# Kernel optimization log

Measured on AMD Instinct MI355X. Metric: run time of the kernel, lower is better.

## Reference

```python
import jax, jax.numpy as jnp
import numpy as np

B, S, I, H, O, L = 64, 1024, 128, 512, 128, 2

def _gru_layer(x, h0, Wzx, Wzh, bz, Wrx, Wrh, br, Wgx, Wgh, bg):
    # Precompute input projections for all timesteps: (B,S,H)
    xz = jnp.einsum('bsi,ih->bsh', x, Wzx)
    xr = jnp.einsum('bsi,ih->bsh', x, Wrx)
    xg = jnp.einsum('bsi,ih->bsh', x, Wgx)
    def step(h, inp):
        xz_t, xr_t, xg_t = inp
        z = jax.nn.sigmoid(xz_t + h @ Wzh + bz)
        r = jax.nn.sigmoid(xr_t + h @ Wrh + br)
        g = jnp.tanh(xg_t + (r * h) @ Wgh + bg)
        h_new = z * h + (1.0 - z) * g
        return h_new, h_new
    # scan over time: move S to leading axis
    xs = (jnp.swapaxes(xz, 0, 1), jnp.swapaxes(xr, 0, 1), jnp.swapaxes(xg, 0, 1))
    hT, ys = jax.lax.scan(step, h0, xs)
    return jnp.swapaxes(ys, 0, 1), hT  # (B,S,H), (B,H)

def setup_inputs() -> dict:
    key = jax.random.key(0)
    ks = jax.random.split(key, 32)
    d = {}
    d['input'] = jax.random.normal(ks[0], (B, S, I), dtype=jnp.float32)
    d['hidden_state'] = jnp.zeros((B, L, H), dtype=jnp.float32)
    kidx = 1
    for layer in range(L):
        din = I if layer == 0 else H
        sx = 1.0 / np.sqrt(din)
        sh = 1.0 / np.sqrt(H)
        for gate in ('z', 'r', 'g'):
            d[f'W{gate}x{layer}'] = jax.random.uniform(ks[kidx], (din, H), jnp.float32, -sx, sx); kidx += 1
            d[f'W{gate}h{layer}'] = jax.random.uniform(ks[kidx], (H, H), jnp.float32, -sh, sh); kidx += 1
            d[f'b{gate}{layer}'] = jax.random.uniform(ks[kidx], (H,), jnp.float32, -sh, sh); kidx += 1
    so = 1.0 / np.sqrt(H)
    d['Wout'] = jax.random.uniform(ks[kidx], (H, O), jnp.float32, -so, so); kidx += 1
    d['bout'] = jax.random.uniform(ks[kidx], (O,), jnp.float32, -so, so)
    return d

def reference(input, hidden_state,
              Wzx0, Wzh0, bz0, Wrx0, Wrh0, br0, Wgx0, Wgh0, bg0,
              Wzx1, Wzh1, bz1, Wrx1, Wrh1, br1, Wgx1, Wgh1, bg1,
              Wout, bout):
    params = [
        (Wzx0, Wzh0, bz0, Wrx0, Wrh0, br0, Wgx0, Wgh0, bg0),
        (Wzx1, Wzh1, bz1, Wrx1, Wrh1, br1, Wgx1, Wgh1, bg1),
    ]
    x = input
    finals = []
    for layer in range(L):
        h0 = hidden_state[:, layer, :]
        x, hT = _gru_layer(x, h0, *params[layer])
        finals.append(hT)
    layer_output = jnp.einsum('bsh,ho->bso', x, Wout) + bout  # (B,S,O)
    hidden_out = jnp.stack(finals, axis=1)  # (B,L,H)
    return layer_output, hidden_out
```

## Files before the change

### kernel.cpp

```cpp
#include <hip/hip_runtime.h>
#include <cstdint>
#include <cstddef>

#define BDIM 256
#define NWG  256

constexpr int B_ = 64, S_ = 1024, I_ = 128, H_ = 512, O_ = 128;
constexpr size_t HB = (size_t)H_ * B_;

constexpr size_t Y1_OFF  = 0;
constexpr size_t Y2_OFF  = Y1_OFF + 2 * HB;
constexpr size_t RH0_OFF = Y2_OFF + 2 * HB;
constexpr size_t RH1_OFF = RH0_OFF + HB;
constexpr size_t Z0_OFF  = RH1_OFF + HB;
constexpr size_t Z1_OFF  = Z0_OFF + HB;
constexpr size_t BAR_OFF = Z1_OFF + HB;
constexpr size_t BAR_WORDS = 34 * 64;
constexpr size_t SLAB_TOT = BAR_OFF + BAR_WORDS;
constexpr size_t XT_OFF  = SLAB_TOT;
constexpr size_t XT_FLOATS = (size_t)S_ * I_ * B_;
constexpr size_t WS_NEED_XT_BYTES = (XT_OFF + XT_FLOATS) * 4;

__device__ __forceinline__ float4 llc_load4(const float* p) {
  const unsigned long long* q = (const unsigned long long*)p;
  unsigned long long lo = __hip_atomic_load(q,     __ATOMIC_RELAXED, __HIP_MEMORY_SCOPE_AGENT);
  unsigned long long hi = __hip_atomic_load(q + 1, __ATOMIC_RELAXED, __HIP_MEMORY_SCOPE_AGENT);
  union { unsigned long long u[2]; float4 v; } c;
  c.u[0] = lo; c.u[1] = hi;
  return c.v;
}
__device__ __forceinline__ float llc_loadf(const float* p) {
  unsigned int u = __hip_atomic_load((const unsigned int*)p, __ATOMIC_RELAXED,
                                     __HIP_MEMORY_SCOPE_AGENT);
  union { unsigned int u; float f; } c; c.u = u;
  return c.f;
}
__device__ __forceinline__ void llc_storef(float* p, float x) {
  union { float f; unsigned int u; } c; c.f = x;
  __hip_atomic_store((unsigned int*)p, c.u, __ATOMIC_RELAXED, __HIP_MEMORY_SCOPE_AGENT);
}

__global__ void k_init(const float* __restrict__ hidden, float* __restrict__ ws) {
  int idx = blockIdx.x * 256 + threadIdx.x;
  if (idx < (int)(2 * HB)) {
    int l = idx >> 15, r = idx & 32767;
    int k = r >> 6, b = r & 63;
    ws[(l ? Y2_OFF : Y1_OFF) + HB + r] = hidden[b * 1024 + l * 512 + k];
  } else if (idx < (int)(2 * HB + BAR_WORDS)) {
    ((unsigned int*)(ws + BAR_OFF))[idx - 2 * HB] = 0u;
  }
}

__global__ void k_transpose_x(const float* __restrict__ in, float* __restrict__ Xt) {
  const size_t NQ = (size_t)B_ * S_ * I_ / 4;
  for (size_t q = (size_t)blockIdx.x * blockDim.x + threadIdx.x; q < NQ;
       q += (size_t)gridDim.x * blockDim.x) {
    int i4 = (int)(q & 31);
    int t  = (int)((q >> 5) & 1023);
    int b  = (int)(q >> 15);
    float4 v = *(const float4*)(in + ((size_t)b * 1024 + t) * 128 + i4 * 4);
    float* dst = Xt + (size_t)t * 8192 + (size_t)(i4 * 4) * 64 + b;
    dst[0] = v.x; dst[64] = v.y; dst[128] = v.z; dst[192] = v.w;
  }
}

__device__ __forceinline__ void fmas(float4& a, float s, const float4 h) {
  a.x = fmaf(s, h.x, a.x); a.y = fmaf(s, h.y, a.y);
  a.z = fmaf(s, h.z, a.z); a.w = fmaf(s, h.w, a.w);
}

__device__ __forceinline__ void dotA8(const float* __restrict__ src, const float* __restrict__ wAp,
                                      int kt, int b4, float4* acc) {
  #pragma unroll 8
  for (int ch = 0; ch < 32; ++ch) {
    int kk = ch * 16 + kt;
    float4 h = llc_load4(src + (size_t)kk * 64 + b4);
    const float* wp = wAp + kk * 8;
    float4 w0 = *(const float4*)wp;
    float4 w1 = *(const float4*)(wp + 4);
    fmas(acc[0], w0.x, h); fmas(acc[1], w0.y, h); fmas(acc[2], w0.z, h); fmas(acc[3], w0.w, h);
    fmas(acc[4], w1.x, h); fmas(acc[5], w1.y, h); fmas(acc[6], w1.z, h); fmas(acc[7], w1.w, h);
  }
}

__device__ __forceinline__ void fusedL1r1(const float* __restrict__ src,
                                          const float* __restrict__ wAp,
                                          const float* __restrict__ wBp,
                                          int kt, int b4, float4* acc, float4* accB) {
  #pragma unroll 8
  for (int ch = 0; ch < 32; ++ch) {
    int kk = ch * 16 + kt;
    float4 h = llc_load4(src + (size_t)kk * 64 + b4);
    const float* wp = wAp + kk * 8;
    float4 w0 = *(const float4*)wp;
    float4 w1 = *(const float4*)(wp + 4);
    fmas(acc[0], w0.x, h); fmas(acc[1], w0.y, h); fmas(acc[2], w0.z, h); fmas(acc[3], w0.w, h);
    fmas(acc[4], w1.x, h); fmas(acc[5], w1.y, h); fmas(acc[6], w1.z, h); fmas(acc[7], w1.w, h);
    const float* gp = wBp + kk * 4;
    float4 g0 = *(const float4*)gp;
    fmas(accB[0], g0.x, h); fmas(accB[1], g0.y, h); fmas(accB[2], g0.z, h); fmas(accB[3], g0.w, h);
  }
}

__device__ __forceinline__ void fusedL1r2(const float* __restrict__ src,
                                          const float* __restrict__ wAp2,
                                          const float* __restrict__ wOp,
                                          int kt, int b4, float4* acc, float4& accO) {
  #pragma unroll 8
  for (int ch = 0; ch < 32; ++ch) {
    int kk = ch * 16 + kt;
    float4 h = llc_load4(src + (size_t)kk * 64 + b4);
    const float* wp = wAp2 + kk * 8;
    float4 w0 = *(const float4*)wp;
    float4 w1 = *(const float4*)(wp + 4);
    fmas(acc[0], w0.x, h); fmas(acc[1], w0.y, h); fmas(acc[2], w0.z, h); fmas(acc[3], w0.w, h);
    fmas(acc[4], w1.x, h); fmas(acc[5], w1.y, h); fmas(acc[6], w1.z, h); fmas(acc[7], w1.w, h);
    fmas(accO, wOp[kk], h);
  }
}

__device__ __forceinline__ void fusedL0x(const float* __restrict__ src,
                                         const float* __restrict__ wAp2,
                                         const float* __restrict__ wBp2,
                                         int kt, int b4, float4* acc, float4* accB) {
  #pragma unroll 8
  for (int ch = 0; ch < 8; ++ch) {
    int i = ch * 16 + kt;
    float4 h = *(const float4*)(src + (size_t)i * 64 + b4);
    const float* wp = wAp2 + i * 8;
    float4 w0 = *(const float4*)wp;
    float4 w1 = *(const float4*)(wp + 4);
    fmas(acc[0], w0.x, h); fmas(acc[1], w0.y, h); fmas(acc[2], w0.z, h); fmas(acc[3], w0.w, h);
    fmas(acc[4], w1.x, h); fmas(acc[5], w1.y, h); fmas(acc[6], w1.z, h); fmas(acc[7], w1.w, h);
    const float* gp = wBp2 + i * 4;
    float4 g0 = *(const float4*)gp;
    fmas(accB[0], g0.x, h); fmas(accB[1], g0.y, h); fmas(accB[2], g0.z, h); fmas(accB[3], g0.w, h);
  }
}

__device__ __forceinline__ void fusedL0xf(const float* __restrict__ xin, int tau,
                                          const float* __restrict__ wAp2,
                                          const float* __restrict__ wBp2,
                                          int kt, int b4, float4* acc, float4* accB) {
  #pragma unroll 2
  for (int ch = 0; ch < 8; ++ch) {
    int i = ch * 16 + kt;
    float4 h;
    h.x = xin[(size_t)(b4 + 0) * 131072 + tau * 128 + i];
    h.y = xin[(size_t)(b4 + 1) * 131072 + tau * 128 + i];
    h.z = xin[(size_t)(b4 + 2) * 131072 + tau * 128 + i];
    h.w = xin[(size_t)(b4 + 3) * 131072 + tau * 128 + i];
    const float* wp = wAp2 + i * 8;
    float4 w0 = *(const float4*)wp;
    float4 w1 = *(const float4*)(wp + 4);
    fmas(acc[0], w0.x, h); fmas(acc[1], w0.y, h); fmas(acc[2], w0.z, h); fmas(acc[3], w0.w, h);
    fmas(acc[4], w1.x, h); fmas(acc[5], w1.y, h); fmas(acc[6], w1.z, h); fmas(acc[7], w1.w, h);
    const float* gp = wBp2 + i * 4;
    float4 g0 = *(const float4*)gp;
    fmas(accB[0], g0.x, h); fmas(accB[1], g0.y, h); fmas(accB[2], g0.z, h); fmas(accB[3], g0.w, h);
  }
}

__device__ __forceinline__ void dotB4(const float* __restrict__ src, const float* __restrict__ wBp,
                                      int kt, int b4, float4* acc) {
  #pragma unroll 8
  for (int ch = 0; ch < 32; ++ch) {
    int kk = ch * 16 + kt;
    float4 h = llc_load4(src + (size_t)kk * 64 + b4);
    const float* wp = wBp + kk * 4;
    float4 w0 = *(const float4*)wp;
    fmas(acc[0], w0.x, h); fmas(acc[1], w0.y, h); fmas(acc[2], w0.z, h); fmas(acc[3], w0.w, h);
  }
}

__device__ __forceinline__ void grid_barrier(unsigned int* bar, unsigned int ph) {
  __syncthreads();
  asm volatile("" ::: "memory");
  if (threadIdx.x == 0) {
    const int g = (int)(blockIdx.x >> 4);
    unsigned int* grp_cnt  = bar + (size_t)g * 64;
    unsigned int* root_cnt = bar + 16 * 64;
    unsigned int* grp_gen  = bar + (size_t)(17 + g) * 64;
    unsigned int* root_gen = bar + 33 * 64;
    unsigned int r = __hip_atomic_fetch_add(grp_cnt, 1u, __ATOMIC_RELAXED, __HIP_MEMORY_SCOPE_AGENT);
    if (r == 16u * ph - 1u) {
      unsigned int rr = __hip_atomic_fetch_add(root_cnt, 1u, __ATOMIC_RELAXED, __HIP_MEMORY_SCOPE_AGENT);
      if (rr == 16u * ph - 1u) {
        __hip_atomic_store(root_gen, ph, __ATOMIC_RELAXED, __HIP_MEMORY_SCOPE_AGENT);
      } else {
        while (__hip_atomic_load(root_gen, __ATOMIC_RELAXED, __HIP_MEMORY_SCOPE_AGENT) < ph)
          __builtin_amdgcn_s_sleep(1);
      }
      __hip_atomic_store(grp_gen, ph, __ATOMIC_RELAXED, __HIP_MEMORY_SCOPE_AGENT);
    } else {
      while (__hip_atomic_load(grp_gen, __ATOMIC_RELAXED, __HIP_MEMORY_SCOPE_AGENT) < ph)
        __builtin_amdgcn_s_sleep(1);
    }
  }
  asm volatile("" ::: "memory");
  __syncthreads();
}

struct ScanArgs {
  float* ws;
  const float* xin;
  float* out;
  const float *Wzx0, *Wzh0, *bz0, *Wrx0, *Wrh0, *br0, *Wgx0, *Wgh0, *bg0;
  const float *Wzx1, *Wzh1, *bz1, *Wrx1, *Wrh1, *br1, *Wgx1, *Wgh1, *bg1;
  const float *Wout, *bout;
  int use_xt;
};

__launch_bounds__(BDIM, 1)
__global__ void k_scan(ScanArgs a) {
  float* ws = a.ws;
  unsigned int* bar = (unsigned int*)(ws + BAR_OFF);

  const int tid = threadIdx.x;
  const int wg  = blockIdx.x;
  const int kt  = tid >> 4;
  const int bq  = tid & 15;
  const int b4  = bq << 2;

  const int mA  = wg >> 6;
  const int lA  = mA >> 1;
  const int gA  = mA & 1;
  const int jA0 = (wg & 63) * 8;
  const int KA  = (mA < 2) ? 640 : 1024;
  const int mB  = wg >> 7;
  const int jB0 = (wg & 127) * 4;
  const int KB  = mB ? 1024 : 640;
  const int oc  = wg - 128;

  __shared__ float wA[8192];
  __shared__ float wB[4096];
  __shared__ float wO[512];
  __shared__ float pA[9 * 64 * 17];

  {
    const float* A0 = lA ? (gA ? a.Wrx1 : a.Wzx1) : (gA ? a.Wrh0 : a.Wzh0);
    const float* A1 = lA ? (gA ? a.Wrh1 : a.Wzh1) : (gA ? a.Wrx0 : a.Wzx0);
    for (int idx = tid; idx < KA * 8; idx += BDIM) {
      int k = idx >> 3, c = idx & 7;
      wA[idx] = (k < 512) ? A0[k * 512 + jA0 + c] : A1[(k - 512) * 512 + jA0 + c];
    }
    const float* B0 = mB ? a.Wgx1 : a.Wgh0;
    const float* B1 = mB ? a.Wgh1 : a.Wgx0;
    for (int idx = tid; idx < KB * 4; idx += BDIM) {
      int k = idx >> 2, c = idx & 3;
      wB[idx] = (k < 512) ? B0[k * 512 + jB0 + c] : B1[(k - 512) * 512 + jB0 + c];
    }
    if (wg >= 128)
      for (int idx = tid; idx < 512; idx += BDIM) wO[idx] = a.Wout[(size_t)idx * 128 + oc];
  }
  const float* bAv = lA ? (gA ? a.br1 : a.bz1) : (gA ? a.br0 : a.bz0);
  const float biasA_0 = bAv[jA0 + (tid >> 6)];
  const float biasA_1 = bAv[jA0 + 4 + (tid >> 6)];
  const float biasB_0 = (mB ? a.bg1 : a.bg0)[jB0 + (tid >> 6)];
  const float boutW = (wg >= 128) ? a.bout[oc] : 0.f;
  __syncthreads();

  const float* XT = ws + XT_OFF;
  unsigned int ph = 1;

  for (int tau = 0; tau <= S_ + 1; ++tau) {
    const bool doL0 = (tau < S_);
    const bool doL1 = (tau >= 1) && (tau <= S_);
    const int slotP = (tau + 1) & 1;
    const int slotQ = tau & 1;
    const float* y1p = ws + Y1_OFF + (size_t)slotP * HB;
    const float* y2p = ws + Y2_OFF + (size_t)slotQ * HB;
    float* y1w = ws + Y1_OFF + (size_t)slotQ * HB;
    float* y2w = ws + Y2_OFF + (size_t)slotP * HB;

    const bool actA = lA ? doL1 : doL0;
    const bool doOut = (tau >= 2) && (wg >= 128);
    float4 acc[8];
    float4 accB[4];
    float4 accO = make_float4(0.f, 0.f, 0.f, 0.f);
    #pragma unroll
    for (int c = 0; c < 8; ++c) acc[c] = make_float4(0.f, 0.f, 0.f, 0.f);
    #pragma unroll
    for (int c = 0; c < 4; ++c) accB[c] = make_float4(0.f, 0.f, 0.f, 0.f);

    if (actA) {
      if (mA < 2) {
        dotA8(y1p, wA, kt, b4, acc);
        if (a.use_xt) fusedL0x(XT + (size_t)tau * 8192, wA + 512 * 8, wB + 512 * 4, kt, b4, acc, accB);
        else          fusedL0xf(a.xin, tau, wA + 512 * 8, wB + 512 * 4, kt, b4, acc, accB);
      } else {
        fusedL1r1(y1p, wA, wB, kt, b4, acc, accB);
        fusedL1r2(y2p, wA + 512 * 8, wO, kt, b4, acc, accO);
      }
    } else if (tau == S_ + 1 && wg >= 128) {
      #pragma unroll 8
      for (int ch = 0; ch < 32; ++ch) {
        int kk = ch * 16 + kt;
        float4 h = llc_load4(y2p + (size_t)kk * 64 + b4);
        fmas(accO, wO[kk], h);
      }
    }

    if (actA) {
      #pragma unroll
      for (int c = 0; c < 8; ++c) {
        float pv[4] = {acc[c].x, acc[c].y, acc[c].z, acc[c].w};
        #pragma unroll
        for (int j = 0; j < 4; ++j) pA[(c * 64 + b4 + j) * 17 + kt] = pv[j];
      }
    }
    if (doOut) {
      float pv[4] = {accO.x, accO.y, accO.z, accO.w};
      #pragma unroll
      for (int j = 0; j < 4; ++j) pA[(512 + b4 + j) * 17 + kt] = pv[j];
    }
    __syncthreads();
    if (actA) {
      #pragma unroll
      for (int r = 0; r < 2; ++r) {
        int idx = tid + (r << 8);
        int c = idx >> 6, b = idx & 63;
        float s = r ? biasA_1 : biasA_0;
        #pragma unroll
        for (int q = 0; q < 16; ++q) s += pA[(c * 64 + b) * 17 + q];
        float v = 1.0f / (1.0f + __expf(-s));
        size_t jb = (size_t)(jA0 + c) * 64 + b;
        if (gA == 0) {
          llc_storef(ws + (lA ? Z1_OFF : Z0_OFF) + jb, v);
        } else {
          const float* hpsl = lA ? y2p : y1p;
          float hp = llc_loadf(hpsl + jb);
          llc_storef(ws + (lA ? RH1_OFF : RH0_OFF) + jb, v * hp);
        }
      }
    }
    if (doOut && tid < 64) {
      float s = boutW;
      #pragma unroll
      for (int q = 0; q < 16; ++q) s += pA[(512 + tid) * 17 + q];
      a.out[((size_t)tid * 1024 + (tau - 2)) * 128 + oc] = s;
    }

    grid_barrier(bar, ph++);

    const bool actB = mB ? doL1 : doL0;
    if (actB) {
      if (mB == 0) dotB4(ws + RH0_OFF, wB, kt, b4, accB);
      else         dotB4(ws + RH1_OFF, wB + 512 * 4, kt, b4, accB);
      #pragma unroll
      for (int c = 0; c < 4; ++c) {
        float pv[4] = {accB[c].x, accB[c].y, accB[c].z, accB[c].w};
        #pragma unroll
        for (int j = 0; j < 4; ++j) pA[(c * 64 + b4 + j) * 17 + kt] = pv[j];
      }
    }
    __syncthreads();
    if (actB) {
      int c = tid >> 6, b = tid & 63;
      float s = biasB_0;
      #pragma unroll
      for (int q = 0; q < 16; ++q) s += pA[(c * 64 + b) * 17 + q];
      float g = tanhf(s);
      size_t jb = (size_t)(jB0 + c) * 64 + b;
      float z  = llc_loadf(ws + (mB ? Z1_OFF : Z0_OFF) + jb);
      float hp = llc_loadf((mB ? y2p : y1p) + jb);
      float hn = fmaf(z, hp - g, g);
      llc_storef((mB ? y2w : y1w) + jb, hn);
    }

    grid_barrier(bar, ph++);
  }
}

__global__ void k_hidden(const float* __restrict__ ws, float* __restrict__ out) {
  int idx = blockIdx.x * 256 + threadIdx.x;
  int b = idx >> 10, rem = idx & 1023, l = rem >> 9, j = rem & 511;
  const float* src = ws + (l ? Y2_OFF : Y1_OFF) + HB + (size_t)j * 64 + b;
  out[(size_t)B_ * S_ * O_ + idx] = *src;
}

extern "C" void kernel_launch(void* const* d_in, const int* in_sizes, int n_in,
                              void* d_out, int out_size, void* d_ws, size_t ws_size,
                              hipStream_t stream) {
  const float* input  = (const float*)d_in[0];
  const float* hidden = (const float*)d_in[1];
  const float* Wzx0 = (const float*)d_in[2],  *Wzh0 = (const float*)d_in[3],  *bz0 = (const float*)d_in[4];
  const float* Wrx0 = (const float*)d_in[5],  *Wrh0 = (const float*)d_in[6],  *br0 = (const float*)d_in[7];
  const float* Wgx0 = (const float*)d_in[8],  *Wgh0 = (const float*)d_in[9],  *bg0 = (const float*)d_in[10];
  const float* Wzx1 = (const float*)d_in[11], *Wzh1 = (const float*)d_in[12], *bz1 = (const float*)d_in[13];
  const float* Wrx1 = (const float*)d_in[14], *Wrh1 = (const float*)d_in[15], *br1 = (const float*)d_in[16];
  const float* Wgx1 = (const float*)d_in[17], *Wgh1 = (const float*)d_in[18], *bg1 = (const float*)d_in[19];
  const float* Wout = (const float*)d_in[20], *bout = (const float*)d_in[21];
  float* ws = (float*)d_ws;
  float* out = (float*)d_out;

  const int use_xt = (ws_size >= WS_NEED_XT_BYTES) ? 1 : 0;

  k_init<<<265, BDIM, 0, stream>>>(hidden, ws);
  if (use_xt) k_transpose_x<<<2048, BDIM, 0, stream>>>(input, ws + XT_OFF);

  ScanArgs sa{ws, input, out,
              Wzx0, Wzh0, bz0, Wrx0, Wrh0, br0, Wgx0, Wgh0, bg0,
              Wzx1, Wzh1, bz1, Wrx1, Wrh1, br1, Wgx1, Wgh1, bg1,
              Wout, bout, use_xt};
  k_scan<<<dim3(NWG), dim3(BDIM), 0, stream>>>(sa);

  k_hidden<<<256, 256, 0, stream>>>(ws, out);
}
```

Measured before the change: 18.28 ms.

## Double scan workgroup threads and pre-reduce K-split partials with wave shuffles

```diff
diff --git a/kernel.cpp b/kernel.cpp
--- a/kernel.cpp
+++ b/kernel.cpp
@@ -2,7 +2,8 @@
 #include <cstdint>
 #include <cstddef>
 
-#define BDIM 256
+#define BDIM 512
+#define ABLK 256
 #define NWG  256
 
 constexpr int B_ = 64, S_ = 1024, I_ = 128, H_ = 512, O_ = 128;
@@ -41,7 +42,7 @@
 }
 
 __global__ void k_init(const float* __restrict__ hidden, float* __restrict__ ws) {
-  int idx = blockIdx.x * 256 + threadIdx.x;
+  int idx = blockIdx.x * ABLK + threadIdx.x;
   if (idx < (int)(2 * HB)) {
     int l = idx >> 15, r = idx & 32767;
     int k = r >> 6, b = r & 63;
@@ -72,8 +73,8 @@
 __device__ __forceinline__ void dotA8(const float* __restrict__ src, const float* __restrict__ wAp,
                                       int kt, int b4, float4* acc) {
   #pragma unroll 8
-  for (int ch = 0; ch < 32; ++ch) {
-    int kk = ch * 16 + kt;
+  for (int ch = 0; ch < 16; ++ch) {
+    int kk = ch * 32 + kt;
     float4 h = llc_load4(src + (size_t)kk * 64 + b4);
     const float* wp = wAp + kk * 8;
     float4 w0 = *(const float4*)wp;
@@ -88,8 +89,8 @@
                                           const float* __restrict__ wBp,
                                           int kt, int b4, float4* acc, float4* accB) {
   #pragma unroll 8
-  for (int ch = 0; ch < 32; ++ch) {
-    int kk = ch * 16 + kt;
+  for (int ch = 0; ch < 16; ++ch) {
+    int kk = ch * 32 + kt;
     float4 h = llc_load4(src + (size_t)kk * 64 + b4);
     const float* wp = wAp + kk * 8;
     float4 w0 = *(const float4*)wp;
@@ -107,8 +108,8 @@
                                           const float* __restrict__ wOp,
                                           int kt, int b4, float4* acc, float4& accO) {
   #pragma unroll 8
-  for (int ch = 0; ch < 32; ++ch) {
-    int kk = ch * 16 + kt;
+  for (int ch = 0; ch < 16; ++ch) {
+    int kk = ch * 32 + kt;
     float4 h = llc_load4(src + (size_t)kk * 64 + b4);
     const float* wp = wAp2 + kk * 8;
     float4 w0 = *(const float4*)wp;
@@ -123,9 +124,9 @@
                                          const float* __restrict__ wAp2,
                                          const float* __restrict__ wBp2,
                                          int kt, int b4, float4* acc, float4* accB) {
-  #pragma unroll 8
-  for (int ch = 0; ch < 8; ++ch) {
-    int i = ch * 16 + kt;
+  #pragma unroll 4
+  for (int ch = 0; ch < 4; ++ch) {
+    int i = ch * 32 + kt;
     float4 h = *(const float4*)(src + (size_t)i * 64 + b4);
     const float* wp = wAp2 + i * 8;
     float4 w0 = *(const float4*)wp;
@@ -143,8 +144,8 @@
                                           const float* __restrict__ wBp2,
                                           int kt, int b4, float4* acc, float4* accB) {
   #pragma unroll 2
-  for (int ch = 0; ch < 8; ++ch) {
-    int i = ch * 16 + kt;
+  for (int ch = 0; ch < 4; ++ch) {
+    int i = ch * 32 + kt;
     float4 h;
     h.x = xin[(size_t)(b4 + 0) * 131072 + tau * 128 + i];
     h.y = xin[(size_t)(b4 + 1) * 131072 + tau * 128 + i];
@@ -164,13 +165,21 @@
 __device__ __forceinline__ void dotB4(const float* __restrict__ src, const float* __restrict__ wBp,
                                       int kt, int b4, float4* acc) {
   #pragma unroll 8
-  for (int ch = 0; ch < 32; ++ch) {
-    int kk = ch * 16 + kt;
+  for (int ch = 0; ch < 16; ++ch) {
+    int kk = ch * 32 + kt;
     float4 h = llc_load4(src + (size_t)kk * 64 + b4);
     const float* wp = wBp + kk * 4;
     float4 w0 = *(const float4*)wp;
     fmas(acc[0], w0.x, h); fmas(acc[1], w0.y, h); fmas(acc[2], w0.z, h); fmas(acc[3], w0.w, h);
   }
+}
+
+__device__ __forceinline__ float4 wave_red4(float4 v) {
+  v.x += __shfl_down(v.x, 32); v.y += __shfl_down(v.y, 32);
+  v.z += __shfl_down(v.z, 32); v.w += __shfl_down(v.w, 32);
+  v.x += __shfl_down(v.x, 16); v.y += __shfl_down(v.y, 16);
+  v.z += __shfl_down(v.z, 16); v.w += __shfl_down(v.w, 16);
+  return v;
 }
 
 __device__ __forceinline__ void grid_barrier(unsigned int* bar, unsigned int ph) {
@@ -221,6 +230,8 @@
   const int kt  = tid >> 4;
   const int bq  = tid & 15;
   const int b4  = bq << 2;
+  const int ktg = kt >> 2;
+  const bool strl = ((kt & 3) == 0);
 
   const int mA  = wg >> 6;
   const int lA  = mA >> 1;
@@ -235,7 +246,7 @@
   __shared__ float wA[8192];
   __shared__ float wB[4096];
   __shared__ float wO[512];
-  __shared__ float pA[9 * 64 * 17];
+  __shared__ float pA[9 * 64 * 9];
 
   {
     const float* A0 = lA ? (gA ? a.Wrx1 : a.Wzx1) : (gA ? a.Wrh0 : a.Wzh0);
@@ -254,9 +265,8 @@
       for (int idx = tid; idx < 512; idx += BDIM) wO[idx] = a.Wout[(size_t)idx * 128 + oc];
   }
   const float* bAv = lA ? (gA ? a.br1 : a.bz1) : (gA ? a.br0 : a.bz0);
-  const float biasA_0 = bAv[jA0 + (tid >> 6)];
-  const float biasA_1 = bAv[jA0 + 4 + (tid >> 6)];
-  const float biasB_0 = (mB ? a.bg1 : a.bg0)[jB0 + (tid >> 6)];
+  const float biasA = bAv[jA0 + (tid >> 6)];
+  const float biasB = (tid < 256) ? (mB ? a.bg1 : a.bg0)[jB0 + (tid >> 6)] : 0.f;
   const float boutW = (wg >= 128) ? a.bout[oc] : 0.f;
   __syncthreads();
 
@@ -294,8 +304,8 @@
       }
     } else if (tau == S_ + 1 && wg >= 128) {
       #pragma unroll 8
-      for (int ch = 0; ch < 32; ++ch) {
-        int kk = ch * 16 + kt;
+      for (int ch = 0; ch < 16; ++ch) {
+        int kk = ch * 32 + kt;
         float4 h = llc_load4(y2p + (size_t)kk * 64 + b4);
         fmas(accO, wO[kk], h);
       }
@@ -304,40 +314,44 @@
     if (actA) {
       #pragma unroll
       for (int c = 0; c < 8; ++c) {
-        float pv[4] = {acc[c].x, acc[c].y, acc[c].z, acc[c].w};
-        #pragma unroll
-        for (int j = 0; j < 4; ++j) pA[(c * 64 + b4 + j) * 17 + kt] = pv[j];
+        float4 v = wave_red4(acc[c]);
+        if (strl) {
+          pA[(c * 64 + b4 + 0) * 9 + ktg] = v.x;
+          pA[(c * 64 + b4 + 1) * 9 + ktg] = v.y;
+          pA[(c * 64 + b4 + 2) * 9 + ktg] = v.z;
+          pA[(c * 64 + b4 + 3) * 9 + ktg] = v.w;
+        }
       }
     }
     if (doOut) {
-      float pv[4] = {accO.x, accO.y, accO.z, accO.w};
-      #pragma unroll
-      for (int j = 0; j < 4; ++j) pA[(512 + b4 + j) * 17 + kt] = pv[j];
+      float4 v = wave_red4(accO);
+      if (strl) {
+        pA[(512 + b4 + 0) * 9 + ktg] = v.x;
+        pA[(512 + b4 + 1) * 9 + ktg] = v.y;
+        pA[(512 + b4 + 2) * 9 + ktg] = v.z;
+        pA[(512 + b4 + 3) * 9 + ktg] = v.w;
+      }
     }
     __syncthreads();
     if (actA) {
+      int c = tid >> 6, b = tid & 63;
+      float s = biasA;
       #pragma unroll
-      for (int r = 0; r < 2; ++r) {
-        int idx = tid + (r << 8);
-        int c = idx >> 6, b = idx & 63;
-        float s = r ? biasA_1 : biasA_0;
-        #pragma unroll
-        for (int q = 0; q < 16; ++q) s += pA[(c * 64 + b) * 17 + q];
-        float v = 1.0f / (1.0f + __expf(-s));
-        size_t jb = (size_t)(jA0 + c) * 64 + b;
-        if (gA == 0) {
-          llc_storef(ws + (lA ? Z1_OFF : Z0_OFF) + jb, v);
-        } else {
-          const float* hpsl = lA ? y2p : y1p;
-          float hp = llc_loadf(hpsl + jb);
-          llc_storef(ws + (lA ? RH1_OFF : RH0_OFF) + jb, v * hp);
-        }
+      for (int q = 0; q < 8; ++q) s += pA[(c * 64 + b) * 9 + q];
+      float v = 1.0f / (1.0f + __expf(-s));
+      size_t jb = (size_t)(jA0 + c) * 64 + b;
+      if (gA == 0) {
+        llc_storef(ws + (lA ? Z1_OFF : Z0_OFF) + jb, v);
+      } else {
+        const float* hpsl = lA ? y2p : y1p;
+        float hp = llc_loadf(hpsl + jb);
+        llc_storef(ws + (lA ? RH1_OFF : RH0_OFF) + jb, v * hp);
       }
     }
     if (doOut && tid < 64) {
       float s = boutW;
       #pragma unroll
-      for (int q = 0; q < 16; ++q) s += pA[(512 + tid) * 17 + q];
+      for (int q = 0; q < 8; ++q) s += pA[(512 + tid) * 9 + q];
       a.out[((size_t)tid * 1024 + (tau - 2)) * 128 + oc] = s;
     }
 
@@ -349,17 +363,21 @@
       else         dotB4(ws + RH1_OFF, wB + 512 * 4, kt, b4, accB);
       #pragma unroll
       for (int c = 0; c < 4; ++c) {
-        float pv[4] = {accB[c].x, accB[c].y, accB[c].z, accB[c].w};
-        #pragma unroll
-        for (int j = 0; j < 4; ++j) pA[(c * 64 + b4 + j) * 17 + kt] = pv[j];
+        float4 v = wave_red4(accB[c]);
+        if (strl) {
+          pA[(c * 64 + b4 + 0) * 9 + ktg] = v.x;
+          pA[(c * 64 + b4 + 1) * 9 + ktg] = v.y;
+          pA[(c * 64 + b4 + 2) * 9 + ktg] = v.z;
+          pA[(c * 64 + b4 + 3) * 9 + ktg] = v.w;
+        }
       }
     }
     __syncthreads();
-    if (actB) {
+    if (actB && tid < 256) {
       int c = tid >> 6, b = tid & 63;
-      float s = biasB_0;
+      float s = biasB;
       #pragma unroll
-      for (int q = 0; q < 16; ++q) s += pA[(c * 64 + b) * 17 + q];
+      for (int q = 0; q < 8; ++q) s += pA[(c * 64 + b) * 9 + q];
       float g = tanhf(s);
       size_t jb = (size_t)(jB0 + c) * 64 + b;
       float z  = llc_loadf(ws + (mB ? Z1_OFF : Z0_OFF) + jb);
@@ -373,7 +391,7 @@
 }
 
 __global__ void k_hidden(const float* __restrict__ ws, float* __restrict__ out) {
-  int idx = blockIdx.x * 256 + threadIdx.x;
+  int idx = blockIdx.x * ABLK + threadIdx.x;
   int b = idx >> 10, rem = idx & 1023, l = rem >> 9, j = rem & 511;
   const float* src = ws + (l ? Y2_OFF : Y1_OFF) + HB + (size_t)j * 64 + b;
   out[(size_t)B_ * S_ * O_ + idx] = *src;
@@ -396,8 +414,8 @@
 
   const int use_xt = (ws_size >= WS_NEED_XT_BYTES) ? 1 : 0;
 
-  k_init<<<265, BDIM, 0, stream>>>(hidden, ws);
-  if (use_xt) k_transpose_x<<<2048, BDIM, 0, stream>>>(input, ws + XT_OFF);
+  k_init<<<265, ABLK, 0, stream>>>(hidden, ws);
+  if (use_xt) k_transpose_x<<<2048, ABLK, 0, stream>>>(input, ws + XT_OFF);
 
   ScanArgs sa{ws, input, out,
               Wzx0, Wzh0, bz0, Wrx0, Wrh0, br0, Wgx0, Wgh0, bg0,
@@ -405,5 +423,5 @@
               Wout, bout, use_xt};
   k_scan<<<dim3(NWG), dim3(BDIM), 0, stream>>>(sa);
 
-  k_hidden<<<256, 256, 0, stream>>>(ws, out);
-}
+  k_hidden<<<256, ABLK, 0, stream>>>(ws, out);
+}
```

After: 19.94 ms. 9.1% more time.
